# Kernel optimization log

Hardware: AMD Instinct MI355X
Metric: run time of the kernel (lower is better)

Reference implementation:

```python
import jax, jax.numpy as jnp
import numpy as np

N = 100000  # nodes
E = 1600000  # edges
D_IN, D_HID, D_OUT = 128, 128, 64
NEG_SLOPE = 0.2


def gat_conv(x, src, dst, W_src, W_dst, att_src, att_dst, bias, num_nodes):
    # PyG GATConv, heads=1, add_self_loops=False.
    h_src = x @ W_src          # [N, C]
    h_dst = x @ W_dst          # [N, C]
    a_src = (h_src * att_src).sum(-1)   # [N]
    a_dst = (h_dst * att_dst).sum(-1)   # [N]
    logits = jax.nn.leaky_relu(a_src[src] + a_dst[dst], NEG_SLOPE)  # [E]
    # segment softmax over destination neighborhoods
    seg_max = jax.ops.segment_max(logits, dst, num_segments=num_nodes)  # [N]
    e = jnp.exp(logits - seg_max[dst])
    denom = jax.ops.segment_sum(e, dst, num_segments=num_nodes)         # [N]
    alpha = e / (denom[dst] + 1e-16)                                    # [E]
    out = jax.ops.segment_sum(alpha[:, None] * h_src[src], dst, num_segments=num_nodes)  # [N, C]
    return out + bias


def setup_inputs() -> dict:
    key = jax.random.key(0)
    ks = jax.random.split(key, 12)
    x = jax.random.normal(ks[0], (N, D_IN), dtype=jnp.float32)
    edge_index = jax.random.randint(ks[1], (2, E), 0, N, dtype=jnp.int64)
    s1 = 1.0 / np.sqrt(D_IN)
    s2 = 1.0 / np.sqrt(D_HID)
    return {
        "x": x,
        "edge_index": edge_index,
        "W1_src": jax.random.uniform(ks[2], (D_IN, D_HID), jnp.float32, -s1, s1),
        "W1_dst": jax.random.uniform(ks[3], (D_IN, D_HID), jnp.float32, -s1, s1),
        "att1_src": jax.random.uniform(ks[4], (D_HID,), jnp.float32, -s2, s2),
        "att1_dst": jax.random.uniform(ks[5], (D_HID,), jnp.float32, -s2, s2),
        "b1": jnp.zeros((D_HID,), jnp.float32),
        "W2_src": jax.random.uniform(ks[6], (D_HID, D_OUT), jnp.float32, -s2, s2),
        "W2_dst": jax.random.uniform(ks[7], (D_HID, D_OUT), jnp.float32, -s2, s2),
        "att2_src": jax.random.uniform(ks[8], (D_OUT,), jnp.float32, -1.0 / np.sqrt(D_OUT), 1.0 / np.sqrt(D_OUT)),
        "att2_dst": jax.random.uniform(ks[9], (D_OUT,), jnp.float32, -1.0 / np.sqrt(D_OUT), 1.0 / np.sqrt(D_OUT)),
        "b2": jnp.zeros((D_OUT,), jnp.float32),
    }


def reference(x, edge_index, W1_src, W1_dst, att1_src, att1_dst, b1,
              W2_src, W2_dst, att2_src, att2_dst, b2):
    src, dst = edge_index[0], edge_index[1]
    h = gat_conv(x, src, dst, W1_src, W1_dst, att1_src, att1_dst, b1, N)
    h = jax.nn.relu(h)
    out = gat_conv(h, src, dst, W2_src, W2_dst, att2_src, att2_dst, b2, N)
    return out
```

## Files before the change

### kernel.cpp

```cpp
#include <hip/hip_runtime.h>


typedef unsigned long long u64;
typedef float v4f __attribute__((ext_vector_type(4)));
typedef _Float16 v2h __attribute__((ext_vector_type(2)));
typedef __fp16 h8 __attribute__((ext_vector_type(8)));

#define SEL_LO 0x01000504u
#define SEL_HI 0x03020706u

__device__ __forceinline__ void ntstore4(float* p, v4f v) {
    __builtin_nontemporal_store(v, (v4f*)p);
}
__device__ __forceinline__ unsigned h2pack(float a, float b) {
    v2h h;
    h.x = (_Float16)a;
    h.y = (_Float16)b;
    return __builtin_bit_cast(unsigned, h);
}
__device__ __forceinline__ float fdot2u(unsigned u, v2h w, float acc) {
    return __builtin_amdgcn_fdot2(__builtin_bit_cast(v2h, u), w, acc, false);
}
__device__ __forceinline__ v2h pkrtz(float a, float b) {
    return __builtin_bit_cast(v2h, __builtin_amdgcn_cvt_pkrtz(a, b));
}

__device__ void matvec_body(const float* __restrict__ W, const float* __restrict__ a,
                            float* __restrict__ out, int cols, int row) {
    int lane = threadIdx.x & 63;
    float s = 0.f;
    for (int j = lane; j < cols; j += 64) s += W[row * cols + j] * a[j];
#pragma unroll
    for (int o = 32; o; o >>= 1) s += __shfl_xor(s, o, 64);
    if (lane == 0) out[row] = s;
}

template <int C>
__device__ void packw_body(const float* __restrict__ W, uint4* __restrict__ Wp) {
    constexpr int NT = C / 16;
    const int total = 4 * NT * 64;
    for (int e = threadIdx.x; e < total; e += 256) {
        int lane = e & 63;
        int ti = (e >> 6) % NT;
        int t = (e >> 6) / NT;
        int k0 = 32 * t + (lane >> 4) * 8;
        int n = ti * 16 + (lane & 15);
        unsigned u[4];
#pragma unroll
        for (int p = 0; p < 4; ++p)
            u[p] = h2pack(W[(size_t)(k0 + 2 * p) * C + n], W[(size_t)(k0 + 2 * p + 1) * C + n]);
        Wp[e] = make_uint4(u[0], u[1], u[2], u[3]);
    }
}

__global__ __launch_bounds__(256) void setup_kernel(
    const int* __restrict__ dst, int* __restrict__ hist, int E, int nbE,
    const float* __restrict__ W1s, uint4* __restrict__ wp1,
    const float* __restrict__ W2s, uint4* __restrict__ wp2,
    const float* __restrict__ W1d, const float* __restrict__ att1d, float* __restrict__ watt1,
    const float* __restrict__ W2d, const float* __restrict__ att2d, float* __restrict__ watt2) {
    int b = blockIdx.x;
    if (b < nbE) {
        __shared__ int h[256];
        h[threadIdx.x] = 0;
        __syncthreads();
        int base = b * 4096;
        int lim = min(base + 4096, E);
        for (int i = base + threadIdx.x; i < lim; i += 256)
            atomicAdd(&h[__builtin_nontemporal_load(dst + i) >> 9], 1);
        __syncthreads();
        __builtin_nontemporal_store(h[threadIdx.x], hist + b * 256 + threadIdx.x);
    } else if (b == nbE) {
        packw_body<128>(W1s, wp1);
    } else if (b == nbE + 1) {
        packw_body<64>(W2s, wp2);
    } else if (b < nbE + 34) {
        matvec_body(W1d, att1d, watt1, 128, (b - nbE - 2) * 4 + (threadIdx.x >> 6));
    } else {
        matvec_body(W2d, att2d, watt2, 64, (b - nbE - 34) * 4 + (threadIdx.x >> 6));
    }
}

__global__ __launch_bounds__(256) void bscan_kernel(const int* __restrict__ hist, int nbE,
                                                    int* __restrict__ bbase,
                                                    int* __restrict__ gcur,
                                                    int* __restrict__ offs, int N, int E) {
    __shared__ int s[256];
    int t = threadIdx.x;
    int v = 0;
#pragma unroll 4
    for (int b = 0; b < nbE; ++b) v += hist[b * 256 + t];
    s[t] = v;
    __syncthreads();
    for (int o = 1; o < 256; o <<= 1) {
        int u = (t >= o) ? s[t - o] : 0;
        __syncthreads();
        s[t] += u;
        __syncthreads();
    }
    int excl = s[t] - v;
    bbase[t] = excl;
    gcur[t] = excl;
    if (t == 255) { bbase[256] = E; offs[N] = E; }
}

__device__ void scatter_body(const int* __restrict__ src, const int* __restrict__ dst,
                             int* __restrict__ gcur, u64* __restrict__ pairs, int E,
                             int blk, char* smem) {
    int* h = (int*)smem;
    int* sbase = h + 256;
    int* rbase = h + 512;
    u64* buf = (u64*)(smem + 3072);
    const int tid = threadIdx.x;
    h[tid] = 0;
    __syncthreads();
    const int base = blk * 4096;
    const int lim = min(4096, E - base);
    u64 pv[16];
    int rk[16];
    int bk[16];
#pragma unroll 16
    for (int k = 0; k < 16; ++k) {
        int i = base + k * 256 + tid;
        if (i < E) {
            int d = __builtin_nontemporal_load(dst + i);
            int b = d >> 9;
            bk[k] = b;
            pv[k] = ((u64)(unsigned)d << 32) | (unsigned)__builtin_nontemporal_load(src + i);
            rk[k] = atomicAdd(&h[b], 1);
        } else {
            bk[k] = -1;
        }
    }
    __syncthreads();
    const int v = h[tid];
    sbase[tid] = v;
    __syncthreads();
    for (int o = 1; o < 256; o <<= 1) {
        int uu = (tid >= o) ? sbase[tid - o] : 0;
        __syncthreads();
        sbase[tid] += uu;
        __syncthreads();
    }
    const int excl = sbase[tid] - v;
    rbase[tid] = v ? atomicAdd(&gcur[tid], v) : 0;
    __syncthreads();
    sbase[tid] = excl;
    __syncthreads();
#pragma unroll 16
    for (int k = 0; k < 16; ++k)
        if (bk[k] >= 0) buf[sbase[bk[k]] + rk[k]] = pv[k];
    __syncthreads();
    for (int i = tid; i < lim; i += 256) {
        u64 p = buf[i];
        int b = (int)(p >> 41);
        __builtin_nontemporal_store(p, pairs + (size_t)rbase[b] + (i - sbase[b]));
    }
}

__global__ __launch_bounds__(512) void bsort_kernel(const u64* __restrict__ pairs,
                                                    const int* __restrict__ bbase,
                                                    int* __restrict__ offs,
                                                    int* __restrict__ srcs, int N) {
    __shared__ int h[512];
    __shared__ int cur[512];
    const int t = threadIdx.x;
    const int b = blockIdx.x;
    const int beg = bbase[b], end = bbase[b + 1];
    h[t] = 0;
    __syncthreads();
    for (int i = beg + t; i < end; i += 512)
        atomicAdd(&h[(int)(__builtin_nontemporal_load(pairs + i) >> 32) & 511], 1);
    __syncthreads();
    int v = h[t];
    cur[t] = v;
    __syncthreads();
    for (int o = 1; o < 512; o <<= 1) {
        int u = (t >= o) ? cur[t - o] : 0;
        __syncthreads();
        cur[t] += u;
        __syncthreads();
    }
    int pos0 = beg + cur[t] - v;
    __syncthreads();
    cur[t] = pos0;
    int g = (b << 9) + t;
    if (g < N) offs[g] = pos0;
    __syncthreads();
    for (int i = beg + t; i < end; i += 512) {
        u64 p = __builtin_nontemporal_load(pairs + i);
        int local = (int)(p >> 32) & 511;
        int pp = atomicAdd(&cur[local], 1);
        srcs[pp] = (int)(p & 0xffffffffu);
    }
}

template <int C, bool XF16>
__device__ void gemm_body(int blk, const void* __restrict__ Xv, const uint4* __restrict__ Wp,
                          const float* __restrict__ attS, const float* __restrict__ wda,
                          unsigned* __restrict__ H, float* __restrict__ aS,
                          float* __restrict__ aD, int M, _Float16* hsAll) {
    constexpr int NT = C / 16;
    const int tid = threadIdx.x;
    const int w = tid >> 6;
    const int lane = tid & 63;
    const int l15 = lane & 15;
    const int q = lane >> 4;
    const int mb = blk * 64 + w * 16;
    const int m = mb + l15;
    const bool mv = m < M;

    v4f acc[NT];
#pragma unroll
    for (int n = 0; n < NT; ++n) acc[n] = (v4f)(0.f);
    float pd = 0.f;
    uint4 afu[4];

    if constexpr (XF16) {
        const uint4* Xp = (const uint4*)Xv + (size_t)m * 16;
#pragma unroll
        for (int t = 0; t < 4; ++t) {
            uint4 u = make_uint4(0u, 0u, 0u, 0u);
            if (mv) u = Xp[4 * t + q];
            afu[t] = u;
            const float* wdp = wda + 32 * t + 8 * q;
            pd = fdot2u(u.x, pkrtz(wdp[0], wdp[1]), pd);
            pd = fdot2u(u.y, pkrtz(wdp[2], wdp[3]), pd);
            pd = fdot2u(u.z, pkrtz(wdp[4], wdp[5]), pd);
            pd = fdot2u(u.w, pkrtz(wdp[6], wdp[7]), pd);
        }
    } else {
        const float* Xp = (const float*)Xv + (size_t)m * 128;
#pragma unroll
        for (int t = 0; t < 4; ++t) {
            float4 x0 = make_float4(0.f, 0.f, 0.f, 0.f);
            float4 x1 = x0;
            if (mv) {
                x0 = *(const float4*)(Xp + 32 * t + 8 * q);
                x1 = *(const float4*)(Xp + 32 * t + 8 * q + 4);
            }
            const float* wdp = wda + 32 * t + 8 * q;
            pd += x0.x * wdp[0] + x0.y * wdp[1] + x0.z * wdp[2] + x0.w * wdp[3] +
                  x1.x * wdp[4] + x1.y * wdp[5] + x1.z * wdp[6] + x1.w * wdp[7];
            afu[t] = make_uint4(h2pack(x0.x, x0.y), h2pack(x0.z, x0.w),
                                h2pack(x1.x, x1.y), h2pack(x1.z, x1.w));
        }
    }

#pragma unroll
    for (int t = 0; t < 4; ++t) {
        h8 a = __builtin_bit_cast(h8, afu[t]);
        const uint4* wp = Wp + (size_t)t * NT * 64 + lane;
#pragma unroll
        for (int n = 0; n < NT; ++n) {
            h8 b = __builtin_bit_cast(h8, wp[n * 64]);
            acc[n] = __builtin_amdgcn_mfma_f32_16x16x32_f16(a, b, acc[n], 0, 0, 0);
        }
    }

    pd += __shfl_xor(pd, 16, 64);
    pd += __shfl_xor(pd, 32, 64);
    if (q == 0 && mv) aD[m] = pd;

    float as4[4] = {0.f, 0.f, 0.f, 0.f};
#pragma unroll
    for (int n = 0; n < NT; ++n) {
        float av = attS[n * 16 + l15];
#pragma unroll
        for (int r = 0; r < 4; ++r) as4[r] += acc[n][r] * av;
    }
#pragma unroll
    for (int r = 0; r < 4; ++r) {
#pragma unroll
        for (int o = 1; o < 16; o <<= 1) as4[r] += __shfl_xor(as4[r], o, 64);
    }
    if (l15 == 0) {
#pragma unroll
        for (int r = 0; r < 4; ++r) {
            int row = mb + q * 4 + r;
            if (row < M) aS[row] = as4[r];
        }
    }

    _Float16* hp = hsAll + w * (16 * 136);
#pragma unroll
    for (int n = 0; n < NT; ++n)
#pragma unroll
        for (int r = 0; r < 4; ++r)
            hp[(q * 4 + r) * 136 + n * 16 + l15] = (_Float16)acc[n][r];

    constexpr int CH = C / 32;
    if (lane < 16 * CH) {
        int row = lane / CH;
        int ch = lane % CH;
        const uint4* rp = (const uint4*)(hp + row * 136 + ch * 32);
        uint4 v0 = rp[0], v1 = rp[1], v2 = rp[2], v3 = rp[3];
        int gr = mb + row;
        if (gr < M) {
            uint4* op = (uint4*)(H + (size_t)gr * (C / 2)) + ch * 4;
            op[0] = v0; op[1] = v1; op[2] = v2; op[3] = v3;
        }
    }
}

template <int C, bool XF16>
__global__ __launch_bounds__(256) void gemm_att_kernel(
    const void* __restrict__ Xv, const uint4* __restrict__ Wp,
    const float* __restrict__ attS, const float* __restrict__ wda,
    unsigned* __restrict__ H, float* __restrict__ aS, float* __restrict__ aD, int M) {
    __shared__ _Float16 hs[4 * 16 * 136];
    gemm_body<C, XF16>(blockIdx.x, Xv, Wp, attS, wda, H, aS, aD, M, hs);
}

__global__ __launch_bounds__(256) void scatter_gemm_kernel(
    const int* __restrict__ src, const int* __restrict__ dst, int* __restrict__ gcur,
    u64* __restrict__ pairs, int E, int nbS,
    const void* __restrict__ Xv, const uint4* __restrict__ Wp,
    const float* __restrict__ attS, const float* __restrict__ wda,
    unsigned* __restrict__ H, float* __restrict__ aS, float* __restrict__ aD, int M) {
    __shared__ __align__(16) char smem[35840];
    int b = blockIdx.x;
    if (b < nbS) scatter_body(src, dst, gcur, pairs, E, b, smem);
    else gemm_body<128, false>(b - nbS, Xv, Wp, attS, wda, H, aS, aD, M, (_Float16*)smem);
}

template <int C, bool RELU, bool F16OUT, bool NTOUT>
__global__ __launch_bounds__(256) void aggregate_kernel(
    const int* __restrict__ offs, const int* __restrict__ srcs,
    const unsigned* __restrict__ hsrc, const float* __restrict__ aS,
    const float* __restrict__ aD, const float* __restrict__ bias,
    void* __restrict__ outv, int n) {
    const int lane = threadIdx.x & 63;
    const int sl = lane & 31;
    const int hb = lane & 32;
    const int g = (lane >> 4) & 1;
    const int l = lane & 15;
    int node = (int)((blockIdx.x * blockDim.x + threadIdx.x) >> 5);
    if (node >= n) return;

    const int beg = offs[node], end = offs[node + 1];
    const int deg = end - beg;
    const float ad = aD[node];

    constexpr int LW = C / 32;
    constexpr int NA = C / 16;
    float acc[NA];
#pragma unroll
    for (int i = 0; i < NA; ++i) acc[i] = 0.f;

    int sj = 0;
    float u = 0.f;

    auto ldrow = [&](int s, unsigned* r) {
        if constexpr (C == 128) {
            uint4 v = ((const uint4*)(hsrc + ((size_t)s << 6)))[l];
            r[0] = v.x; r[1] = v.y; r[2] = v.z; r[3] = v.w;
        } else {
            uint2 v = ((const uint2*)(hsrc + ((size_t)s << 5)))[l];
            r[0] = v.x; r[1] = v.y;
        }
    };
    auto issue = [&](int j, unsigned (*buf)[LW]) {
        int e0 = hb + j * 8 + g;
        int s0 = __shfl(sj, e0, 64);
        int s1 = __shfl(sj, e0 + 2, 64);
        int s2 = __shfl(sj, e0 + 4, 64);
        int s3 = __shfl(sj, e0 + 6, 64);
        ldrow(s0, buf[0]);
        ldrow(s1, buf[1]);
        ldrow(s2, buf[2]);
        ldrow(s3, buf[3]);
    };
    auto compute = [&](int j, unsigned (*buf)[LW], float inv) {
        int e0 = hb + j * 8 + g;
        float w0 = __shfl(u, e0, 64) * inv, w1 = __shfl(u, e0 + 2, 64) * inv;
        float w2 = __shfl(u, e0 + 4, 64) * inv, w3 = __shfl(u, e0 + 6, 64) * inv;
        v2h w01 = pkrtz(w0, w1);
        v2h w23 = pkrtz(w2, w3);
#pragma unroll
        for (int ii = 0; ii < LW; ++ii) {
            acc[2 * ii] = fdot2u(__builtin_amdgcn_perm(buf[0][ii], buf[1][ii], SEL_LO), w01,
                          fdot2u(__builtin_amdgcn_perm(buf[2][ii], buf[3][ii], SEL_LO), w23, acc[2 * ii]));
            acc[2 * ii + 1] = fdot2u(__builtin_amdgcn_perm(buf[0][ii], buf[1][ii], SEL_HI), w01,
                              fdot2u(__builtin_amdgcn_perm(buf[2][ii], buf[3][ii], SEL_HI), w23, acc[2 * ii + 1]));
        }
    };

    unsigned A0[4][LW], A1[4][LW];

    if (deg <= 32) {
        int i = beg + sl;
        if (i < end) {
            sj = __builtin_nontemporal_load(srcs + i);
            float lg = aS[sj] + ad;
            lg = (lg > 0.f) ? lg : 0.2f * lg;
            u = __expf(lg);
        }
        int jm = (deg + 7) >> 3;
        if (jm > 0) issue(0, A0);
        if (jm > 1) issue(1, A1);
        float s = u;
#pragma unroll
        for (int o = 16; o; o >>= 1) s += __shfl_xor(s, o, 64);
        float inv = 1.f / (s + 1e-16f);
        if (jm > 0) { compute(0, A0, inv); if (jm > 2) issue(2, A0); }
        if (jm > 1) { compute(1, A1, inv); if (jm > 3) issue(3, A1); }
        if (jm > 2) compute(2, A0, inv);
        if (jm > 3) compute(3, A1, inv);
    } else {
        float m = -INFINITY;
        for (int i = beg + sl; i < end; i += 32) {
            float lg = aS[srcs[i]] + ad;
            lg = (lg > 0.f) ? lg : 0.2f * lg;
            m = fmaxf(m, lg);
        }
#pragma unroll
        for (int o = 16; o; o >>= 1) m = fmaxf(m, __shfl_xor(m, o, 64));
        float ssum = 0.f;
        for (int i = beg + sl; i < end; i += 32) {
            float lg = aS[srcs[i]] + ad;
            lg = (lg > 0.f) ? lg : 0.2f * lg;
            ssum += __expf(lg - m);
        }
#pragma unroll
        for (int o = 16; o; o >>= 1) ssum += __shfl_xor(ssum, o, 64);
        float inv = 1.f / (ssum + 1e-16f);
        for (int base = beg; base < end; base += 32) {
            int i = base + sl;
            sj = 0;
            u = 0.f;
            if (i < end) {
                sj = srcs[i];
                float lg = aS[sj] + ad;
                lg = (lg > 0.f) ? lg : 0.2f * lg;
                u = __expf(lg - m);
            }
            int cnt = min(32, end - base);
            int cj = (cnt + 7) >> 3;
            if (cj > 0) issue(0, A0);
            if (cj > 1) issue(1, A1);
            if (cj > 0) { compute(0, A0, inv); if (cj > 2) issue(2, A0); }
            if (cj > 1) { compute(1, A1, inv); if (cj > 3) issue(3, A1); }
            if (cj > 2) compute(2, A0, inv);
            if (cj > 3) compute(3, A1, inv);
        }
    }

#pragma unroll
    for (int i = 0; i < NA; ++i) acc[i] += __shfl_xor(acc[i], 16, 64);

    if (sl < 16) {
        float o[NA];
        const float* bp = bias + l * NA;
#pragma unroll
        for (int i = 0; i < NA; ++i) {
            o[i] = acc[i] + bp[i];
            if (RELU) o[i] = fmaxf(o[i], 0.f);
        }
        if constexpr (F16OUT) {
            unsigned uo[NA / 2];
#pragma unroll
            for (int k = 0; k < NA / 2; ++k) uo[k] = h2pack(o[2 * k], o[2 * k + 1]);
            unsigned* op = (unsigned*)outv + (size_t)node * (C / 2) + l * (NA / 2);
            if constexpr (NA == 8) *(uint4*)op = make_uint4(uo[0], uo[1], uo[2], uo[3]);
            else *(uint2*)op = make_uint2(uo[0], uo[1]);
        } else {
            float* op = (float*)outv + (size_t)node * C + l * NA;
#pragma unroll
            for (int q = 0; q < NA / 4; ++q) {
                v4f ov;
                ov.x = o[q * 4 + 0]; ov.y = o[q * 4 + 1];
                ov.z = o[q * 4 + 2]; ov.w = o[q * 4 + 3];
                if (NTOUT) ntstore4(op + q * 4, ov);
                else *(v4f*)(op + q * 4) = ov;
            }
        }
    }
}

extern "C" void kernel_launch(void* const* d_in, const int* in_sizes, int n_in,
                              void* d_out, int out_size, void* d_ws, size_t ws_size,
                              hipStream_t stream) {
    const float* x     = (const float*)d_in[0];
    const int*   edge  = (const int*)d_in[1];
    const float* W1s   = (const float*)d_in[2];
    const float* W1d   = (const float*)d_in[3];
    const float* att1s = (const float*)d_in[4];
    const float* att1d = (const float*)d_in[5];
    const float* b1    = (const float*)d_in[6];
    const float* W2s   = (const float*)d_in[7];
    const float* W2d   = (const float*)d_in[8];
    const float* att2s = (const float*)d_in[9];
    const float* att2d = (const float*)d_in[10];
    const float* b2    = (const float*)d_in[11];

    const int N = in_sizes[0] / 128;
    const int E = in_sizes[1] / 2;
    const int* srcI = edge;
    const int* dstI = edge + E;

    const int nbE = (E + 4095) / 4096;
    const int nbuckets = (N + 511) >> 9;
    const int gblk = (N + 63) / 64;

    size_t off = 0;
    auto alloc = [&](size_t bytes) {
        void* p = (char*)d_ws + off;
        off += (bytes + 255) & ~(size_t)255;
        return p;
    };
    int*      offs  = (int*)alloc((size_t)(N + 1) * 4);
    int*      srcs  = (int*)alloc((size_t)E * 4);
    int*      hist  = (int*)alloc((size_t)nbE * 256 * 4);
    int*      bbase = (int*)alloc(257 * 4);
    int*      gcur  = (int*)alloc(256 * 4);
    float*    watt1 = (float*)alloc(128 * 4);
    float*    watt2 = (float*)alloc(128 * 4);
    uint4*    wp1   = (uint4*)alloc(4 * 8 * 64 * 16);
    uint4*    wp2   = (uint4*)alloc(4 * 4 * 64 * 16);
    float*    a_s   = (float*)alloc((size_t)N * 4);
    float*    a_d   = (float*)alloc((size_t)N * 4);
    unsigned* g1h   = (unsigned*)alloc((size_t)N * 128 * 2);
    unsigned* h1h   = (unsigned*)alloc((size_t)N * 128 * 2);
    unsigned* g2h   = (unsigned*)alloc((size_t)N * 64 * 2);
    u64*      pairs = (u64*)h1h;

    setup_kernel<<<nbE + 66, 256, 0, stream>>>(dstI, hist, E, nbE, W1s, wp1, W2s, wp2,
                                               W1d, att1d, watt1, W2d, att2d, watt2);
    bscan_kernel<<<1, 256, 0, stream>>>(hist, nbE, bbase, gcur, offs, N, E);
    scatter_gemm_kernel<<<nbE + gblk, 256, 0, stream>>>(srcI, dstI, gcur, pairs, E, nbE,
                                                        x, wp1, att1s, watt1, g1h, a_s, a_d, N);
    bsort_kernel<<<nbuckets, 512, 0, stream>>>(pairs, bbase, offs, srcs, N);
    aggregate_kernel<128, true, true, false><<<(N + 7) / 8, 256, 0, stream>>>(
        offs, srcs, g1h, a_s, a_d, b1, h1h, N);
    gemm_att_kernel<64, true><<<gblk, 256, 0, stream>>>(h1h, wp2, att2s, watt2, g2h, a_s, a_d, N);
    aggregate_kernel<64, false, false, true><<<(N + 7) / 8, 256, 0, stream>>>(
        offs, srcs, g2h, a_s, a_d, b2, d_out, N);
}
```

Baseline: 316.6 us.

## Fuse layer-1 aggregation with layer-2 GEMM through shared memory

Replaces the layer-1 aggregate kernel and the layer-2 GEMM/attention kernel with one kernel. Each block aggregates 64 nodes, keeps the ReLU'd fp16 hidden rows in LDS, and runs the MFMA projection and attention dot products on them directly. This removes the global write and re-read of the N×128 hidden tensor and drops one kernel launch. In exchange, each block walks its 64 nodes in 8 sequential steps, which cuts the number of blocks and may hide gather latency less well. The layer-2 attention scores now go to separate buffers, and the edge-pair scratch is aliased onto the layer-2 feature buffer.

```diff
diff --git a/kernel.cpp b/kernel.cpp
--- a/kernel.cpp
+++ b/kernel.cpp
@@ -301,15 +301,6 @@
             op[0] = v0; op[1] = v1; op[2] = v2; op[3] = v3;
         }
     }
-}
-
-template <int C, bool XF16>
-__global__ __launch_bounds__(256) void gemm_att_kernel(
-    const void* __restrict__ Xv, const uint4* __restrict__ Wp,
-    const float* __restrict__ attS, const float* __restrict__ wda,
-    unsigned* __restrict__ H, float* __restrict__ aS, float* __restrict__ aD, int M) {
-    __shared__ _Float16 hs[4 * 16 * 136];
-    gemm_body<C, XF16>(blockIdx.x, Xv, Wp, attS, wda, H, aS, aD, M, hs);
 }
 
 __global__ __launch_bounds__(256) void scatter_gemm_kernel(
@@ -478,6 +469,228 @@
     }
 }
 
+__global__ __launch_bounds__(256) void agg_gemm_kernel(
+    const int* __restrict__ offs, const int* __restrict__ srcs,
+    const unsigned* __restrict__ hsrc, const float* __restrict__ aS,
+    const float* __restrict__ aD, const float* __restrict__ bias,
+    const uint4* __restrict__ Wp2, const float* __restrict__ attS2,
+    const float* __restrict__ wda2, unsigned* __restrict__ g2h,
+    float* __restrict__ aS2, float* __restrict__ aD2, int n) {
+    __shared__ __align__(16) _Float16 lds[64 * 136];
+    const int tid = threadIdx.x;
+    const int lane = tid & 63;
+    const int sl = lane & 31;
+    const int hb = lane & 32;
+    const int g = (lane >> 4) & 1;
+    const int l = lane & 15;
+    const int nodeBase = blockIdx.x * 64;
+
+    if (nodeBase + 64 > n) {
+        for (int i = tid; i < 64 * 136 / 2; i += 256) ((unsigned*)lds)[i] = 0u;
+        __syncthreads();
+    }
+
+    constexpr int LW = 4;
+    constexpr int NA = 8;
+
+    for (int k = 0; k < 8; ++k) {
+        const int node = nodeBase + k * 8 + (tid >> 5);
+        if (node < n) {
+            const int beg = offs[node], end = offs[node + 1];
+            const int deg = end - beg;
+            const float ad = aD[node];
+            float acc[NA];
+#pragma unroll
+            for (int i = 0; i < NA; ++i) acc[i] = 0.f;
+            int sj = 0;
+            float u = 0.f;
+
+            auto ldrow = [&](int s, unsigned* r) {
+                uint4 v = ((const uint4*)(hsrc + ((size_t)s << 6)))[l];
+                r[0] = v.x; r[1] = v.y; r[2] = v.z; r[3] = v.w;
+            };
+            auto issue = [&](int j, unsigned (*buf)[LW]) {
+                int e0 = hb + j * 8 + g;
+                int s0 = __shfl(sj, e0, 64);
+                int s1 = __shfl(sj, e0 + 2, 64);
+                int s2 = __shfl(sj, e0 + 4, 64);
+                int s3 = __shfl(sj, e0 + 6, 64);
+                ldrow(s0, buf[0]);
+                ldrow(s1, buf[1]);
+                ldrow(s2, buf[2]);
+                ldrow(s3, buf[3]);
+            };
+            auto compute = [&](int j, unsigned (*buf)[LW], float inv) {
+                int e0 = hb + j * 8 + g;
+                float w0 = __shfl(u, e0, 64) * inv, w1 = __shfl(u, e0 + 2, 64) * inv;
+                float w2 = __shfl(u, e0 + 4, 64) * inv, w3 = __shfl(u, e0 + 6, 64) * inv;
+                v2h w01 = pkrtz(w0, w1);
+                v2h w23 = pkrtz(w2, w3);
+#pragma unroll
+                for (int ii = 0; ii < LW; ++ii) {
+                    acc[2 * ii] = fdot2u(__builtin_amdgcn_perm(buf[0][ii], buf[1][ii], SEL_LO), w01,
+                                  fdot2u(__builtin_amdgcn_perm(buf[2][ii], buf[3][ii], SEL_LO), w23, acc[2 * ii]));
+                    acc[2 * ii + 1] = fdot2u(__builtin_amdgcn_perm(buf[0][ii], buf[1][ii], SEL_HI), w01,
+                                     fdot2u(__builtin_amdgcn_perm(buf[2][ii], buf[3][ii], SEL_HI), w23, acc[2 * ii + 1]));
+                }
+            };
+
+            unsigned A0[4][LW], A1[4][LW];
+
+            if (deg <= 32) {
+                int i = beg + sl;
+                if (i < end) {
+                    sj = __builtin_nontemporal_load(srcs + i);
+                    float lg = aS[sj] + ad;
+                    lg = (lg > 0.f) ? lg : 0.2f * lg;
+                    u = __expf(lg);
+                }
+                int jm = (deg + 7) >> 3;
+                if (jm > 0) issue(0, A0);
+                if (jm > 1) issue(1, A1);
+                float s = u;
+#pragma unroll
+                for (int o = 16; o; o >>= 1) s += __shfl_xor(s, o, 64);
+                float inv = 1.f / (s + 1e-16f);
+                if (jm > 0) { compute(0, A0, inv); if (jm > 2) issue(2, A0); }
+                if (jm > 1) { compute(1, A1, inv); if (jm > 3) issue(3, A1); }
+                if (jm > 2) compute(2, A0, inv);
+                if (jm > 3) compute(3, A1, inv);
+            } else {
+                float m = -INFINITY;
+                for (int i = beg + sl; i < end; i += 32) {
+                    float lg = aS[srcs[i]] + ad;
+                    lg = (lg > 0.f) ? lg : 0.2f * lg;
+                    m = fmaxf(m, lg);
+                }
+#pragma unroll
+                for (int o = 16; o; o >>= 1) m = fmaxf(m, __shfl_xor(m, o, 64));
+                float ssum = 0.f;
+                for (int i = beg + sl; i < end; i += 32) {
+                    float lg = aS[srcs[i]] + ad;
+                    lg = (lg > 0.f) ? lg : 0.2f * lg;
+                    ssum += __expf(lg - m);
+                }
+#pragma unroll
+                for (int o = 16; o; o >>= 1) ssum += __shfl_xor(ssum, o, 64);
+                float inv = 1.f / (ssum + 1e-16f);
+                for (int base = beg; base < end; base += 32) {
+                    int i = base + sl;
+                    sj = 0;
+                    u = 0.f;
+                    if (i < end) {
+                        sj = srcs[i];
+                        float lg = aS[sj] + ad;
+                        lg = (lg > 0.f) ? lg : 0.2f * lg;
+                        u = __expf(lg - m);
+                    }
+                    int cnt = min(32, end - base);
+                    int cj = (cnt + 7) >> 3;
+                    if (cj > 0) issue(0, A0);
+                    if (cj > 1) issue(1, A1);
+                    if (cj > 0) { compute(0, A0, inv); if (cj > 2) issue(2, A0); }
+                    if (cj > 1) { compute(1, A1, inv); if (cj > 3) issue(3, A1); }
+                    if (cj > 2) compute(2, A0, inv);
+                    if (cj > 3) compute(3, A1, inv);
+                }
+            }
+
+#pragma unroll
+            for (int i = 0; i < NA; ++i) acc[i] += __shfl_xor(acc[i], 16, 64);
+
+            if (sl < 16) {
+                float o[NA];
+                const float* bp = bias + l * NA;
+#pragma unroll
+                for (int i = 0; i < NA; ++i) o[i] = fmaxf(acc[i] + bp[i], 0.f);
+                unsigned uo[4];
+#pragma unroll
+                for (int kk = 0; kk < 4; ++kk) uo[kk] = h2pack(o[2 * kk], o[2 * kk + 1]);
+                unsigned* op = (unsigned*)(lds + (size_t)(k * 8 + (tid >> 5)) * 136) + l * 4;
+                *(uint4*)op = make_uint4(uo[0], uo[1], uo[2], uo[3]);
+            }
+        }
+    }
+    __syncthreads();
+
+    const int w = tid >> 6;
+    const int l15 = lane & 15;
+    const int q = lane >> 4;
+    const int mb = nodeBase + w * 16;
+    const int m = mb + l15;
+    const bool mv = m < n;
+    const _Float16* xrow = lds + (size_t)(w * 16 + l15) * 136;
+
+    v4f acc2[4];
+#pragma unroll
+    for (int nn = 0; nn < 4; ++nn) acc2[nn] = (v4f)(0.f);
+    float pd = 0.f;
+    uint4 afu[4];
+#pragma unroll
+    for (int t = 0; t < 4; ++t) {
+        uint4 u = ((const uint4*)xrow)[4 * t + q];
+        afu[t] = u;
+        const float* wdp = wda2 + 32 * t + 8 * q;
+        pd = fdot2u(u.x, pkrtz(wdp[0], wdp[1]), pd);
+        pd = fdot2u(u.y, pkrtz(wdp[2], wdp[3]), pd);
+        pd = fdot2u(u.z, pkrtz(wdp[4], wdp[5]), pd);
+        pd = fdot2u(u.w, pkrtz(wdp[6], wdp[7]), pd);
+    }
+#pragma unroll
+    for (int t = 0; t < 4; ++t) {
+        h8 a = __builtin_bit_cast(h8, afu[t]);
+        const uint4* wp = Wp2 + (size_t)t * 4 * 64 + lane;
+#pragma unroll
+        for (int nn = 0; nn < 4; ++nn) {
+            h8 b = __builtin_bit_cast(h8, wp[nn * 64]);
+            acc2[nn] = __builtin_amdgcn_mfma_f32_16x16x32_f16(a, b, acc2[nn], 0, 0, 0);
+        }
+    }
+
+    pd += __shfl_xor(pd, 16, 64);
+    pd += __shfl_xor(pd, 32, 64);
+    if (q == 0 && mv) aD2[m] = pd;
+
+    float as4[4] = {0.f, 0.f, 0.f, 0.f};
+#pragma unroll
+    for (int nn = 0; nn < 4; ++nn) {
+        float av = attS2[nn * 16 + l15];
+#pragma unroll
+        for (int r = 0; r < 4; ++r) as4[r] += acc2[nn][r] * av;
+    }
+#pragma unroll
+    for (int r = 0; r < 4; ++r) {
+#pragma unroll
+        for (int o = 1; o < 16; o <<= 1) as4[r] += __shfl_xor(as4[r], o, 64);
+    }
+    if (l15 == 0) {
+#pragma unroll
+        for (int r = 0; r < 4; ++r) {
+            int row = mb + q * 4 + r;
+            if (row < n) aS2[row] = as4[r];
+        }
+    }
+
+    _Float16* hp = lds + (size_t)w * (16 * 136);
+#pragma unroll
+    for (int nn = 0; nn < 4; ++nn)
+#pragma unroll
+        for (int r = 0; r < 4; ++r)
+            hp[(q * 4 + r) * 136 + nn * 16 + l15] = (_Float16)acc2[nn][r];
+
+    if (lane < 32) {
+        int row = lane >> 1;
+        int ch = lane & 1;
+        const uint4* rp = (const uint4*)(hp + row * 136 + ch * 32);
+        uint4 v0 = rp[0], v1 = rp[1], v2 = rp[2], v3 = rp[3];
+        int gr = mb + row;
+        if (gr < n) {
+            uint4* op = (uint4*)(g2h + (size_t)gr * 32) + ch * 4;
+            op[0] = v0; op[1] = v1; op[2] = v2; op[3] = v3;
+        }
+    }
+}
+
 extern "C" void kernel_launch(void* const* d_in, const int* in_sizes, int n_in,
                               void* d_out, int out_size, void* d_ws, size_t ws_size,
                               hipStream_t stream) {
@@ -520,10 +733,11 @@
     uint4*    wp2   = (uint4*)alloc(4 * 4 * 64 * 16);
     float*    a_s   = (float*)alloc((size_t)N * 4);
     float*    a_d   = (float*)alloc((size_t)N * 4);
+    float*    a_s2  = (float*)alloc((size_t)N * 4);
+    float*    a_d2  = (float*)alloc((size_t)N * 4);
     unsigned* g1h   = (unsigned*)alloc((size_t)N * 128 * 2);
-    unsigned* h1h   = (unsigned*)alloc((size_t)N * 128 * 2);
     unsigned* g2h   = (unsigned*)alloc((size_t)N * 64 * 2);
-    u64*      pairs = (u64*)h1h;
+    u64*      pairs = (u64*)g2h;
 
     setup_kernel<<<nbE + 66, 256, 0, stream>>>(dstI, hist, E, nbE, W1s, wp1, W2s, wp2,
                                                W1d, att1d, watt1, W2d, att2d, watt2);
@@ -531,9 +745,8 @@
     scatter_gemm_kernel<<<nbE + gblk, 256, 0, stream>>>(srcI, dstI, gcur, pairs, E, nbE,
                                                         x, wp1, att1s, watt1, g1h, a_s, a_d, N);
     bsort_kernel<<<nbuckets, 512, 0, stream>>>(pairs, bbase, offs, srcs, N);
-    aggregate_kernel<128, true, true, false><<<(N + 7) / 8, 256, 0, stream>>>(
-        offs, srcs, g1h, a_s, a_d, b1, h1h, N);
-    gemm_att_kernel<64, true><<<gblk, 256, 0, stream>>>(h1h, wp2, att2s, watt2, g2h, a_s, a_d, N);
+    agg_gemm_kernel<<<gblk, 256, 0, stream>>>(offs, srcs, g1h, a_s, a_d, b1,
+                                              wp2, att2s, watt2, g2h, a_s2, a_d2, N);
     aggregate_kernel<64, false, false, true><<<(N + 7) / 8, 256, 0, stream>>>(
-        offs, srcs, g2h, a_s, a_d, b2, d_out, N);
-}
+        offs, srcs, g2h, a_s2, a_d2, b2, d_out, N);
+}
```

New measurement: 321.3 us. Within noise of the previous version (+1.5%).
